# Performance work log

Measured on AMD Instinct MI355X. Metric: run time of the kernel, lower is better.

## Reference

```python
import jax, jax.numpy as jnp
import numpy as np

B, T, C = 4, 2048, 1024
H = 16
HD = C // H  # 64


def setup_inputs() -> dict:
    key = jax.random.key(0)
    k1, k2, k3 = jax.random.split(key, 3)
    x = jax.random.normal(k1, (B, T, C), dtype=jnp.float32)
    W_attn = jax.random.normal(k2, (C, 3 * C), dtype=jnp.float32) * (1.0 / np.sqrt(C))
    b_attn = jnp.zeros((3 * C,), dtype=jnp.float32)
    W_proj = jax.random.normal(k3, (C, C), dtype=jnp.float32) * (1.0 / np.sqrt(C))
    b_proj = jnp.zeros((C,), dtype=jnp.float32)
    return {"x": x, "W_attn": W_attn, "b_attn": b_attn, "W_proj": W_proj, "b_proj": b_proj}


def reference(x, W_attn, b_attn, W_proj, b_proj):
    Bx, Tx, Cx = x.shape
    qkv = x @ W_attn + b_attn                      # [B,T,3C]
    q, k, v = jnp.split(qkv, 3, axis=-1)
    # [B,T,C] -> [B,H,T,HD]
    q = q.reshape(Bx, Tx, H, HD).transpose(0, 2, 1, 3)
    k = k.reshape(Bx, Tx, H, HD).transpose(0, 2, 1, 3)
    v = v.reshape(Bx, Tx, H, HD).transpose(0, 2, 1, 3)
    att = jnp.einsum('bhqd,bhkd->bhqk', q, k) / jnp.sqrt(jnp.float32(HD))
    causal = jnp.tril(jnp.ones((Tx, Tx), dtype=bool))
    att = jnp.where(causal[None, None], att, -jnp.inf)
    att = jax.nn.softmax(att, axis=-1)
    y = jnp.einsum('bhqk,bhkd->bhqd', att, v)      # [B,H,T,HD]
    y = y.transpose(0, 2, 1, 3).reshape(Bx, Tx, Cx)
    return y @ W_proj + b_proj
```

## Files before the change

### kernel.cpp

```cpp
#include <hip/hip_runtime.h>
#include <hip/hip_bf16.h>

typedef unsigned short u16;
typedef __attribute__((ext_vector_type(8))) short bf16x8;
typedef __attribute__((ext_vector_type(4))) float f32x4;

#define MFMA16(a, b, c) __builtin_amdgcn_mfma_f32_16x16x32_bf16((a), (b), (c), 0, 0, 0)

__device__ __forceinline__ u16 f2bf(float f) {
  union { float f; unsigned u; } v; v.f = f;
  unsigned r = v.u + 0x7fffu + ((v.u >> 16) & 1u);
  return (u16)(r >> 16);
}

__device__ __forceinline__ unsigned pk_trunc(float hi, float lo) {
  union { float f; unsigned u; } a, b; a.f = hi; b.f = lo;
  return __builtin_amdgcn_perm(a.u, b.u, 0x07060302u);
}

__device__ __forceinline__ void gload_lds16(const u16* g, u16* l) {
  __builtin_amdgcn_global_load_lds((const __attribute__((address_space(1))) void*)g,
                                   (__attribute__((address_space(3))) void*)l, 16, 0, 0);
}

__global__ __launch_bounds__(256) void convert_bf16_k(const float* __restrict__ in,
                                                      u16* __restrict__ out, int n) {
  int i = (blockIdx.x * 256 + threadIdx.x) * 8;
  if (i >= n) return;
  float4 v0 = *(const float4*)(in + i);
  float4 v1 = *(const float4*)(in + i + 4);
  uint4 o;
  o.x = (unsigned)f2bf(v0.x) | ((unsigned)f2bf(v0.y) << 16);
  o.y = (unsigned)f2bf(v0.z) | ((unsigned)f2bf(v0.w) << 16);
  o.z = (unsigned)f2bf(v1.x) | ((unsigned)f2bf(v1.y) << 16);
  o.w = (unsigned)f2bf(v1.z) | ((unsigned)f2bf(v1.w) << 16);
  *(uint4*)(out + i) = o;
}

__global__ __launch_bounds__(256) void transpose2_k(const float* __restrict__ Wa, u16* __restrict__ WaT,
                                                    const float* __restrict__ Wp, u16* __restrict__ WpT) {
  __shared__ float tile[64][65];
  int b = blockIdx.x;
  const float* W; u16* Wt; int N, n0, k0;
  if (b < 768) { W = Wa; Wt = WaT; N = 3072; n0 = (b % 48) * 64; k0 = (b / 48) * 64; }
  else { int c = b - 768; W = Wp; Wt = WpT; N = 1024; n0 = (c & 15) * 64; k0 = (c >> 4) * 64; }
  const int tx = threadIdx.x & 63, ty = threadIdx.x >> 6;
#pragma unroll
  for (int i = 0; i < 16; ++i)
    tile[ty + 4 * i][tx] = W[(size_t)(k0 + ty + 4 * i) * N + n0 + tx];
  __syncthreads();
#pragma unroll
  for (int i = 0; i < 16; ++i)
    Wt[(size_t)(n0 + ty + 4 * i) * 1024 + k0 + tx] = f2bf(tile[tx][ty + 4 * i]);
}

#define BAR() asm volatile("s_barrier" ::: "memory")
#define WLG()                                                   \
  do {                                                          \
    asm volatile("s_waitcnt lgkmcnt(0)" ::: "memory");          \
    __builtin_amdgcn_sched_barrier(0);                          \
  } while (0)
#define VMW(N) asm volatile("s_waitcnt vmcnt(" #N ")" ::: "memory")

#define RING_LANE_CONSTS                                                    \
  const int tid = threadIdx.x, w = tid >> 6, lane = tid & 63;               \
  const int wm = w >> 2, wn = w & 3;                                        \
  const int fr = lane & 15, fg = lane >> 4;                                 \
  const int sr = lane >> 2;                                                 \
  const int sk = (lane & 1) * 8 + ((((lane >> 1) ^ (lane >> 5)) & 1) << 4); \
  const int lsw = fr * 32 + ((fg * 8) ^ ((fr & 8) ? 16 : 0));

__global__ __launch_bounds__(512, 2) void gemm_qkv_r4(const u16* __restrict__ A,
                                                      const u16* __restrict__ Bt,
                                                      const float* __restrict__ bias,
                                                      u16* __restrict__ Qo, u16* __restrict__ Ko,
                                                      u16* __restrict__ Vt) {
  __shared__ u16 sm[4][16384];
  const int bid = blockIdx.x;
  const int swz = (bid & 7) * 48 + (bid >> 3);
  const int m0 = (swz / 12) * 256, n0 = (swz % 12) * 256;
  RING_LANE_CONSTS
  const int aoff = wm * 4096 + lsw;
  const int boff = 8192 + wn * 2048 + lsw;

  const u16* gAw = A + (size_t)(m0 + sr) * 1024 + sk + (size_t)w * 16384;
  const u16* gBw = Bt + (size_t)(n0 + sr) * 1024 + sk + (size_t)w * 16384;

#define QSTG_A(SL, C, KO) \
  gload_lds16(gAw + (size_t)(C) * 131072 + (KO), &sm[SL][(C) * 4096 + w * 512 + lane * 8])
#define QSTG_B(SL, C, KO) \
  gload_lds16(gBw + (size_t)(C) * 131072 + (KO), &sm[SL][8192 + (C) * 4096 + w * 512 + lane * 8])

  f32x4 acc[8][4];
#pragma unroll
  for (int i = 0; i < 8; ++i)
#pragma unroll
    for (int j = 0; j < 4; ++j) acc[i][j] = (f32x4){0, 0, 0, 0};

  QSTG_A(0, 0, 0);  QSTG_B(0, 0, 0);  QSTG_A(0, 1, 0);  QSTG_B(0, 1, 0);
  QSTG_A(1, 0, 32); QSTG_B(1, 0, 32); QSTG_A(1, 1, 32); QSTG_B(1, 1, 32);
  QSTG_A(2, 0, 64); QSTG_B(2, 0, 64); QSTG_A(2, 1, 64); QSTG_B(2, 1, 64);
  int kofs = 96;
  VMW(8); BAR();

#define QLD_A(SL, M0_)                                                    \
  _Pragma("unroll") for (int i = 0; i < 4; ++i)                           \
      av[i] = *(const bf16x8*)&sm[SL][aoff + ((M0_) + i) * 512];
#define QLD_B(SL)                                                         \
  _Pragma("unroll") for (int i = 0; i < 4; ++i)                           \
      bv[i] = *(const bf16x8*)&sm[SL][boff + i * 512];
#define QMM(MB0)                                                          \
  __builtin_amdgcn_s_setprio(1);                                          \
  _Pragma("unroll") for (int i = 0; i < 4; ++i)                           \
      _Pragma("unroll") for (int j = 0; j < 4; ++j)                       \
          acc[(MB0) + i][j] = MFMA16(av[i], bv[j], acc[(MB0) + i][j]);    \
  __builtin_amdgcn_s_setprio(0);

#define QTILE(SL, SS, STG, CHK)                                                \
  {                                                                            \
    bf16x8 av[4], bv[4];                                                       \
    if (STG) { QSTG_A(SS, 0, kofs); QSTG_B(SS, 0, kofs);                       \
               QSTG_A(SS, 1, kofs); QSTG_B(SS, 1, kofs); }                     \
    QLD_A(SL, 0) QLD_B(SL)                                                     \
    WLG(); QMM(0)                                                              \
    QLD_A(SL, 4)                                                               \
    WLG(); QMM(4)                                                              \
    CHK;                                                                       \
    BAR();                                                                     \
    kofs += 32;                                                                \
  }

#pragma unroll 1
  for (int tp = 0; tp < 7; ++tp) {
    QTILE(0, 3, 1, VMW(8)) QTILE(1, 0, 1, VMW(8)) QTILE(2, 1, 1, VMW(8)) QTILE(3, 2, 1, VMW(8))
  }
  QTILE(0, 3, 1, VMW(8))
  QTILE(1, 0, 0, VMW(4))
  QTILE(2, 0, 0, VMW(0))
  QTILE(3, 0, 0, (void)0)

  const int which = n0 >> 10;
  if (which == 2) {
#pragma unroll
    for (int nb = 0; nb < 4; ++nb) {
      const int n = n0 + wn * 64 + nb * 16 + fr;
      const float bs = bias[n];
      const int c = n & 1023, h = c >> 6, hd = c & 63;
#pragma unroll
      for (int mb = 0; mb < 8; ++mb) {
        const int mbase = m0 + wm * 128 + mb * 16 + fg * 4;
        const int bb = mbase >> 11;
        const int tt = mbase & 2047;
        ushort4 pv;
        pv.x = f2bf(acc[mb][nb][0] + bs);
        pv.y = f2bf(acc[mb][nb][1] + bs);
        pv.z = f2bf(acc[mb][nb][2] + bs);
        pv.w = f2bf(acc[mb][nb][3] + bs);
        *(ushort4*)(Vt + ((size_t)(bb * 16 + h) * 64 + hd) * 2048 + tt) = pv;
      }
    }
  } else {
    u16* buf = &sm[0][0];
    const float sc = (which == 0) ? 0.125f : 1.0f;
    u16* outp = (which == 0) ? Qo : Ko;
    float bs4[4];
#pragma unroll
    for (int nb = 0; nb < 4; ++nb) bs4[nb] = bias[n0 + wn * 64 + nb * 16 + fr];
#pragma unroll
    for (int p = 0; p < 2; ++p) {
#pragma unroll
      for (int mb4 = 0; mb4 < 4; ++mb4) {
#pragma unroll
        for (int nb = 0; nb < 4; ++nb) {
#pragma unroll
          for (int r = 0; r < 4; ++r) {
            const int rl = wm * 64 + mb4 * 16 + fg * 4 + r;
            const int col = (wn * 64 + nb * 16 + fr) ^ ((rl & 7) << 3);
            buf[rl * 256 + col] = f2bf((acc[p * 4 + mb4][nb][r] + bs4[nb]) * sc);
          }
        }
      }
      BAR();
      {
        const int rl = tid >> 2, c4 = (tid & 3) * 64;
        const int m = m0 + (rl >> 6) * 128 + p * 64 + (rl & 63);
        const int bb = m >> 11, tt = m & 2047;
        const int n = n0 + c4;
        const int h = (n & 1023) >> 6;
        u16* dst = outp + ((size_t)(bb * 16 + h) * 2048 + tt) * 64;
#pragma unroll
        for (int i = 0; i < 8; ++i) {
          const int col = (c4 + i * 8) ^ ((rl & 7) << 3);
          *(uint4*)(dst + i * 8) = *(const uint4*)&buf[rl * 256 + col];
        }
      }
      BAR();
    }
  }
#undef QSTG_A
#undef QSTG_B
#undef QLD_A
#undef QLD_B
#undef QMM
#undef QTILE
}

__global__ __launch_bounds__(512, 2) void gemm_proj_r4(const u16* __restrict__ A,
                                                       const u16* __restrict__ Bt,
                                                       const float* __restrict__ bias,
                                                       float* __restrict__ O) {
  __shared__ u16 sm[4][12288];
  const int bid = blockIdx.x;
  const int swz = (bid & 7) * 32 + (bid >> 3);
  const int m0 = (swz >> 3) * 256, n0 = (swz & 7) * 128;
  RING_LANE_CONSTS
  const int aoff = wm * 4096 + lsw;
  const int boff = 8192 + wn * 1024 + lsw;

  const u16* gAw = A + (size_t)(m0 + sr) * 1024 + sk + (size_t)w * 16384;
  const u16* gBw = Bt + (size_t)(n0 + sr) * 1024 + sk + (size_t)w * 16384;

#define PSTG_A(SL, C, KO) \
  gload_lds16(gAw + (size_t)(C) * 131072 + (KO), &sm[SL][(C) * 4096 + w * 512 + lane * 8])
#define PSTG_B(SL, KO) \
  gload_lds16(gBw + (KO), &sm[SL][8192 + w * 512 + lane * 8])

  f32x4 acc[8][2];
#pragma unroll
  for (int i = 0; i < 8; ++i)
#pragma unroll
    for (int j = 0; j < 2; ++j) acc[i][j] = (f32x4){0, 0, 0, 0};

  PSTG_A(0, 0, 0);  PSTG_B(0, 0);  PSTG_A(0, 1, 0);
  PSTG_A(1, 0, 32); PSTG_B(1, 32); PSTG_A(1, 1, 32);
  PSTG_A(2, 0, 64); PSTG_B(2, 64); PSTG_A(2, 1, 64);
  int kofs = 96;
  VMW(6); BAR();

#define PLD_A(SL, M0_)                                                    \
  _Pragma("unroll") for (int i = 0; i < 4; ++i)                           \
      av[i] = *(const bf16x8*)&sm[SL][aoff + ((M0_) + i) * 512];
#define PLD_B(SL)                                                         \
  _Pragma("unroll") for (int i = 0; i < 2; ++i)                           \
      bv[i] = *(const bf16x8*)&sm[SL][boff + i * 512];
#define PMM(MB0)                                                          \
  __builtin_amdgcn_s_setprio(1);                                          \
  _Pragma("unroll") for (int i = 0; i < 4; ++i)                           \
      _Pragma("unroll") for (int j = 0; j < 2; ++j)                       \
          acc[(MB0) + i][j] = MFMA16(av[i], bv[j], acc[(MB0) + i][j]);    \
  __builtin_amdgcn_s_setprio(0);

#define PTILE(SL, SS, STG, CHK)                                                \
  {                                                                            \
    bf16x8 av[4], bv[2];                                                       \
    if (STG) { PSTG_A(SS, 0, kofs); PSTG_B(SS, kofs); PSTG_A(SS, 1, kofs); }   \
    PLD_A(SL, 0) PLD_B(SL)                                                     \
    WLG(); PMM(0)                                                              \
    PLD_A(SL, 4)                                                               \
    WLG(); PMM(4)                                                              \
    CHK;                                                                       \
    BAR();                                                                     \
    kofs += 32;                                                                \
  }

#pragma unroll 1
  for (int tp = 0; tp < 7; ++tp) {
    PTILE(0, 3, 1, VMW(6)) PTILE(1, 0, 1, VMW(6)) PTILE(2, 1, 1, VMW(6)) PTILE(3, 2, 1, VMW(6))
  }
  PTILE(0, 3, 1, VMW(6))
  PTILE(1, 0, 0, VMW(3))
  PTILE(2, 0, 0, VMW(0))
  PTILE(3, 0, 0, (void)0)

#pragma unroll
  for (int nb = 0; nb < 2; ++nb) {
    const int n = n0 + wn * 32 + nb * 16 + fr;
    const float bs = bias[n];
#pragma unroll
    for (int mb = 0; mb < 8; ++mb) {
      const int tg = m0 + wm * 128 + mb * 16 + fg * 4;
#pragma unroll
      for (int r = 0; r < 4; ++r) O[(size_t)(tg + r) * 1024 + n] = acc[mb][nb][r] + bs;
    }
  }
#undef PSTG_A
#undef PSTG_B
#undef PLD_A
#undef PLD_B
#undef PMM
#undef PTILE
}

#define PSTR 72
__global__ __launch_bounds__(256) void attn_k(const u16* __restrict__ Q,
                                              const u16* __restrict__ Kb,
                                              const u16* __restrict__ Vt,
                                              u16* __restrict__ Y) {
  __shared__ u16 Ks[64 * 72];
  __shared__ u16 Vs[64 * 72];
  __shared__ u16 Ps[4 * 32 * PSTR];
  const int L = blockIdx.x;
  const int xcd = L & 7, slot = L >> 3;
  const int bh = xcd * 8 + (slot & 7);
  const int i2 = slot >> 3;
  const int qt = (i2 & 4) ? ((i2 & 8) ? 4 + (i2 & 3) : (i2 & 3))
                          : ((i2 & 8) ? 11 - (i2 & 3) : 15 - (i2 & 3));
  const int tid = threadIdx.x, w = tid >> 6, lane = tid & 63;
  const int fr = lane & 15, fg = lane >> 4;
  const u16* Qp = Q + (size_t)bh * 2048 * 64;
  const u16* Kp = Kb + (size_t)bh * 2048 * 64;
  const u16* Vp = Vt + (size_t)bh * 64 * 2048;
  const int qw = qt * 128 + w * 32;

  bf16x8 qa[2][2];
#pragma unroll
  for (int g = 0; g < 2; ++g)
#pragma unroll
    for (int c = 0; c < 2; ++c)
      qa[g][c] = *(const bf16x8*)(Qp + (size_t)(qw + g * 16 + fr) * 64 + c * 32 + fg * 8);

  float li[2] = {0.f, 0.f};
  f32x4 ot[2][4];
#pragma unroll
  for (int g = 0; g < 2; ++g)
#pragma unroll
    for (int mb = 0; mb < 4; ++mb) ot[g][mb] = (f32x4){0, 0, 0, 0};

  const int srow = tid >> 2, scol = (tid & 3) * 16;
  u16* Pw = Ps + w * 32 * PSTR;
  const int nk = 2 * qt + 2;
  const u16* Kg = Kp + (size_t)srow * 64 + scol;
  const u16* Vg = Vp + (size_t)srow * 2048 + scol;

  uint4 kr0 = *(const uint4*)(Kg);
  uint4 kr1 = *(const uint4*)(Kg + 8);
  uint4 vr0 = *(const uint4*)(Vg);
  uint4 vr1 = *(const uint4*)(Vg + 8);

  for (int jt = 0; jt < nk; ++jt) {
    const int k0 = jt * 64;
    if (jt) __syncthreads();
    *(uint4*)&Ks[srow * 72 + scol] = kr0;
    *(uint4*)&Ks[srow * 72 + scol + 8] = kr1;
    *(uint4*)&Vs[srow * 72 + scol] = vr0;
    *(uint4*)&Vs[srow * 72 + scol + 8] = vr1;
    __syncthreads();
    if (jt + 1 < nk) {
      const int kn = (jt + 1) * 64;
      kr0 = *(const uint4*)(Kg + (size_t)kn * 64);
      kr1 = *(const uint4*)(Kg + (size_t)kn * 64 + 8);
      vr0 = *(const uint4*)(Vg + kn);
      vr1 = *(const uint4*)(Vg + kn + 8);
    }
    if (k0 > qw + 31) continue;

    bf16x8 kb[4][2];
#pragma unroll
    for (int nb = 0; nb < 4; ++nb) {
      kb[nb][0] = *(const bf16x8*)&Ks[(nb * 16 + fr) * 72 + fg * 8];
      kb[nb][1] = *(const bf16x8*)&Ks[(nb * 16 + fr) * 72 + 32 + fg * 8];
    }
    f32x4 st[2][4];
    __builtin_amdgcn_s_setprio(1);
#pragma unroll
    for (int g = 0; g < 2; ++g)
#pragma unroll
      for (int nb = 0; nb < 4; ++nb) {
        f32x4 z = (f32x4){0, 0, 0, 0};
        z = MFMA16(kb[nb][0], qa[g][0], z);
        z = MFMA16(kb[nb][1], qa[g][1], z);
        st[g][nb] = z;
      }
    __builtin_amdgcn_s_setprio(0);
    const bool needmask = (k0 + 63 > qw);
#pragma unroll
    for (int g = 0; g < 2; ++g) {
      const int q = qw + g * 16 + fr;
      float rs0 = 0.f, rs1 = 0.f;
#pragma unroll
      for (int nb = 0; nb < 4; ++nb) {
        const int kcb = k0 + nb * 16 + 4 * fg;
        float p0 = __expf(st[g][nb][0]);
        float p1 = __expf(st[g][nb][1]);
        float p2 = __expf(st[g][nb][2]);
        float p3 = __expf(st[g][nb][3]);
        if (needmask) {
          p0 = (kcb + 0 > q) ? 0.f : p0;
          p1 = (kcb + 1 > q) ? 0.f : p1;
          p2 = (kcb + 2 > q) ? 0.f : p2;
          p3 = (kcb + 3 > q) ? 0.f : p3;
        }
        rs0 += p0 + p1;
        rs1 += p2 + p3;
        *(uint2*)&Pw[(g * 16 + fr) * PSTR + nb * 16 + 4 * fg] =
            make_uint2(pk_trunc(p1, p0), pk_trunc(p3, p2));
      }
      li[g] += rs0 + rs1;
    }
    bf16x8 pa[2][2];
#pragma unroll
    for (int g = 0; g < 2; ++g)
#pragma unroll
      for (int H = 0; H < 2; ++H)
        pa[g][H] = *(const bf16x8*)&Pw[(g * 16 + fr) * PSTR + H * 32 + fg * 8];
    __builtin_amdgcn_s_setprio(1);
#pragma unroll
    for (int mb = 0; mb < 4; ++mb) {
      bf16x8 vb0 = *(const bf16x8*)&Vs[(mb * 16 + fr) * 72 + fg * 8];
      bf16x8 vb1 = *(const bf16x8*)&Vs[(mb * 16 + fr) * 72 + 32 + fg * 8];
#pragma unroll
      for (int g = 0; g < 2; ++g) {
        ot[g][mb] = MFMA16(vb0, pa[g][0], ot[g][mb]);
        ot[g][mb] = MFMA16(vb1, pa[g][1], ot[g][mb]);
      }
    }
    __builtin_amdgcn_s_setprio(0);
  }

  const int b = bh >> 4, h = bh & 15;
#pragma unroll
  for (int g = 0; g < 2; ++g) {
    float l = li[g];
    l += __shfl_xor(l, 16);
    l += __shfl_xor(l, 32);
    const float inv = 1.0f / l;
    const int t = qw + g * 16 + fr;
    u16* yrow = Y + ((size_t)b * 2048 + t) * 1024 + h * 64;
#pragma unroll
    for (int mb = 0; mb < 4; ++mb) {
      const unsigned d0 = (unsigned)f2bf(ot[g][mb][0] * inv) |
                          ((unsigned)f2bf(ot[g][mb][1] * inv) << 16);
      const unsigned d1 = (unsigned)f2bf(ot[g][mb][2] * inv) |
                          ((unsigned)f2bf(ot[g][mb][3] * inv) << 16);
      *(uint2*)&yrow[mb * 16 + fg * 4] = make_uint2(d0, d1);
    }
  }
}

extern "C" void kernel_launch(void* const* d_in, const int* in_sizes, int n_in,
                              void* d_out, int out_size, void* d_ws, size_t ws_size,
                              hipStream_t stream) {
  const float* x = (const float*)d_in[0];
  const float* Wa = (const float*)d_in[1];
  const float* ba = (const float*)d_in[2];
  const float* Wp = (const float*)d_in[3];
  const float* bp = (const float*)d_in[4];
  float* out = (float*)d_out;

  char* p = (char*)d_ws;
  u16* xb = (u16*)p;   p += (size_t)8192 * 1024 * 2;
  u16* WaT = (u16*)p;  p += (size_t)3072 * 1024 * 2;
  u16* WpT = (u16*)p;  p += (size_t)1024 * 1024 * 2;
  u16* Qb = (u16*)p;   p += (size_t)64 * 2048 * 64 * 2;
  u16* Kbuf = (u16*)p; p += (size_t)64 * 2048 * 64 * 2;
  u16* Vtb = (u16*)p;  p += (size_t)64 * 64 * 2048 * 2;
  u16* Yb = (u16*)p;   p += (size_t)8192 * 1024 * 2;

  convert_bf16_k<<<4096, 256, 0, stream>>>(x, xb, 8192 * 1024);
  transpose2_k<<<1024, 256, 0, stream>>>(Wa, WaT, Wp, WpT);
  gemm_qkv_r4<<<384, 512, 0, stream>>>(xb, WaT, ba, Qb, Kbuf, Vtb);
  attn_k<<<1024, 256, 0, stream>>>(Qb, Kbuf, Vtb, Yb);
  gemm_proj_r4<<<256, 512, 0, stream>>>(Yb, WpT, bp, out);
}
```

Measured before the change: 240.6 us.

## Retile QKV GEMM to 128x256 blocks with 4 waves and 3-stage ring

The QKV projection GEMM moves from 256x256 tiles with 8 waves and a 4-slot LDS ring to 128x256 tiles with 4 waves, each wave covering a 128x64 strip, and a 3-slot ring. The grid grows from 384 to 768 blocks to improve load balance across CUs, and LDS per block shrinks so more blocks can be resident. The epilogue is simplified to a single LDS staging pass. The cost is lower data reuse per block, since each block now loads more bytes per FLOP, plus a shallower prefetch ring.

```diff
diff --git a/kernel.cpp b/kernel.cpp
--- a/kernel.cpp
+++ b/kernel.cpp
@@ -62,34 +62,29 @@
   } while (0)
 #define VMW(N) asm volatile("s_waitcnt vmcnt(" #N ")" ::: "memory")
 
-#define RING_LANE_CONSTS                                                    \
-  const int tid = threadIdx.x, w = tid >> 6, lane = tid & 63;               \
-  const int wm = w >> 2, wn = w & 3;                                        \
-  const int fr = lane & 15, fg = lane >> 4;                                 \
-  const int sr = lane >> 2;                                                 \
-  const int sk = (lane & 1) * 8 + ((((lane >> 1) ^ (lane >> 5)) & 1) << 4); \
-  const int lsw = fr * 32 + ((fg * 8) ^ ((fr & 8) ? 16 : 0));
-
-__global__ __launch_bounds__(512, 2) void gemm_qkv_r4(const u16* __restrict__ A,
+__global__ __launch_bounds__(256, 2) void gemm_qkv_cr(const u16* __restrict__ A,
                                                       const u16* __restrict__ Bt,
                                                       const float* __restrict__ bias,
                                                       u16* __restrict__ Qo, u16* __restrict__ Ko,
                                                       u16* __restrict__ Vt) {
-  __shared__ u16 sm[4][16384];
+  __shared__ u16 sm[3][12288];
   const int bid = blockIdx.x;
-  const int swz = (bid & 7) * 48 + (bid >> 3);
-  const int m0 = (swz / 12) * 256, n0 = (swz % 12) * 256;
-  RING_LANE_CONSTS
-  const int aoff = wm * 4096 + lsw;
-  const int boff = 8192 + wn * 2048 + lsw;
-
-  const u16* gAw = A + (size_t)(m0 + sr) * 1024 + sk + (size_t)w * 16384;
-  const u16* gBw = Bt + (size_t)(n0 + sr) * 1024 + sk + (size_t)w * 16384;
-
-#define QSTG_A(SL, C, KO) \
-  gload_lds16(gAw + (size_t)(C) * 131072 + (KO), &sm[SL][(C) * 4096 + w * 512 + lane * 8])
-#define QSTG_B(SL, C, KO) \
-  gload_lds16(gBw + (size_t)(C) * 131072 + (KO), &sm[SL][8192 + (C) * 4096 + w * 512 + lane * 8])
+  const int swz = (bid & 7) * 96 + (bid >> 3);
+  const int m0 = (swz / 12) * 128, n0 = (swz % 12) * 256;
+  const int tid = threadIdx.x, w = tid >> 6, lane = tid & 63;
+  const int fr = lane & 15, fg = lane >> 4;
+  const int sk = (tid & 1) * 8 + ((((tid >> 1) ^ (tid >> 5)) & 1) << 4);
+  const int lsw = fr * 32 + ((fg * 8) ^ ((fr & 8) ? 16 : 0));
+  const int aoff = lsw;
+  const int boff = 4096 + w * 2048 + lsw;
+
+  const u16* gA = A + (size_t)(m0 + (tid >> 2)) * 1024 + sk;
+  const u16* gB = Bt + (size_t)(n0 + (tid >> 2)) * 1024 + sk;
+
+#define QSTG_A(SL, C) \
+  gload_lds16(gA + (size_t)(C) * 65536 + kofs, &sm[SL][(C) * 2048 + tid * 8])
+#define QSTG_B(SL, C) \
+  gload_lds16(gB + (size_t)(C) * 65536 + kofs, &sm[SL][4096 + (C) * 2048 + tid * 8])
 
   f32x4 acc[8][4];
 #pragma unroll
@@ -97,11 +92,14 @@
 #pragma unroll
     for (int j = 0; j < 4; ++j) acc[i][j] = (f32x4){0, 0, 0, 0};
 
-  QSTG_A(0, 0, 0);  QSTG_B(0, 0, 0);  QSTG_A(0, 1, 0);  QSTG_B(0, 1, 0);
-  QSTG_A(1, 0, 32); QSTG_B(1, 0, 32); QSTG_A(1, 1, 32); QSTG_B(1, 1, 32);
-  QSTG_A(2, 0, 64); QSTG_B(2, 0, 64); QSTG_A(2, 1, 64); QSTG_B(2, 1, 64);
-  int kofs = 96;
-  VMW(8); BAR();
+  int kofs = 0;
+  QSTG_A(0, 0); QSTG_A(0, 1);
+  QSTG_B(0, 0); QSTG_B(0, 1); QSTG_B(0, 2); QSTG_B(0, 3);
+  kofs = 32;
+  QSTG_A(1, 0); QSTG_A(1, 1);
+  QSTG_B(1, 0); QSTG_B(1, 1); QSTG_B(1, 2); QSTG_B(1, 3);
+  kofs = 64;
+  VMW(6); BAR();
 
 #define QLD_A(SL, M0_)                                                    \
   _Pragma("unroll") for (int i = 0; i < 4; ++i)                           \
@@ -119,8 +117,8 @@
 #define QTILE(SL, SS, STG, CHK)                                                \
   {                                                                            \
     bf16x8 av[4], bv[4];                                                       \
-    if (STG) { QSTG_A(SS, 0, kofs); QSTG_B(SS, 0, kofs);                       \
-               QSTG_A(SS, 1, kofs); QSTG_B(SS, 1, kofs); }                     \
+    if (STG) { QSTG_A(SS, 0); QSTG_A(SS, 1);                                   \
+               QSTG_B(SS, 0); QSTG_B(SS, 1); QSTG_B(SS, 2); QSTG_B(SS, 3); }   \
     QLD_A(SL, 0) QLD_B(SL)                                                     \
     WLG(); QMM(0)                                                              \
     QLD_A(SL, 4)                                                               \
@@ -131,24 +129,22 @@
   }
 
 #pragma unroll 1
-  for (int tp = 0; tp < 7; ++tp) {
-    QTILE(0, 3, 1, VMW(8)) QTILE(1, 0, 1, VMW(8)) QTILE(2, 1, 1, VMW(8)) QTILE(3, 2, 1, VMW(8))
-  }
-  QTILE(0, 3, 1, VMW(8))
-  QTILE(1, 0, 0, VMW(4))
-  QTILE(2, 0, 0, VMW(0))
-  QTILE(3, 0, 0, (void)0)
+  for (int tp = 0; tp < 10; ++tp) {
+    QTILE(0, 2, 1, VMW(6)) QTILE(1, 0, 1, VMW(6)) QTILE(2, 1, 1, VMW(6))
+  }
+  QTILE(0, 0, 0, VMW(0))
+  QTILE(1, 0, 0, (void)0)
 
   const int which = n0 >> 10;
   if (which == 2) {
 #pragma unroll
     for (int nb = 0; nb < 4; ++nb) {
-      const int n = n0 + wn * 64 + nb * 16 + fr;
+      const int n = n0 + w * 64 + nb * 16 + fr;
       const float bs = bias[n];
       const int c = n & 1023, h = c >> 6, hd = c & 63;
 #pragma unroll
       for (int mb = 0; mb < 8; ++mb) {
-        const int mbase = m0 + wm * 128 + mb * 16 + fg * 4;
+        const int mbase = m0 + mb * 16 + fg * 4;
         const int bb = mbase >> 11;
         const int tt = mbase & 2047;
         ushort4 pv;
@@ -165,36 +161,33 @@
     u16* outp = (which == 0) ? Qo : Ko;
     float bs4[4];
 #pragma unroll
-    for (int nb = 0; nb < 4; ++nb) bs4[nb] = bias[n0 + wn * 64 + nb * 16 + fr];
-#pragma unroll
-    for (int p = 0; p < 2; ++p) {
-#pragma unroll
-      for (int mb4 = 0; mb4 < 4; ++mb4) {
-#pragma unroll
-        for (int nb = 0; nb < 4; ++nb) {
-#pragma unroll
-          for (int r = 0; r < 4; ++r) {
-            const int rl = wm * 64 + mb4 * 16 + fg * 4 + r;
-            const int col = (wn * 64 + nb * 16 + fr) ^ ((rl & 7) << 3);
-            buf[rl * 256 + col] = f2bf((acc[p * 4 + mb4][nb][r] + bs4[nb]) * sc);
-          }
+    for (int nb = 0; nb < 4; ++nb) bs4[nb] = bias[n0 + w * 64 + nb * 16 + fr];
+#pragma unroll
+    for (int mb = 0; mb < 8; ++mb) {
+#pragma unroll
+      for (int nb = 0; nb < 4; ++nb) {
+#pragma unroll
+        for (int r = 0; r < 4; ++r) {
+          const int rl = mb * 16 + fg * 4 + r;
+          const int col = (w * 64 + nb * 16 + fr) ^ ((rl & 7) << 3);
+          buf[rl * 256 + col] = f2bf((acc[mb][nb][r] + bs4[nb]) * sc);
         }
       }
-      BAR();
-      {
-        const int rl = tid >> 2, c4 = (tid & 3) * 64;
-        const int m = m0 + (rl >> 6) * 128 + p * 64 + (rl & 63);
-        const int bb = m >> 11, tt = m & 2047;
-        const int n = n0 + c4;
-        const int h = (n & 1023) >> 6;
-        u16* dst = outp + ((size_t)(bb * 16 + h) * 2048 + tt) * 64;
-#pragma unroll
-        for (int i = 0; i < 8; ++i) {
-          const int col = (c4 + i * 8) ^ ((rl & 7) << 3);
-          *(uint4*)(dst + i * 8) = *(const uint4*)&buf[rl * 256 + col];
-        }
-      }
-      BAR();
+    }
+    BAR();
+#pragma unroll
+    for (int p2 = 0; p2 < 2; ++p2) {
+      const int rl = p2 * 64 + (tid >> 2), c4 = (tid & 3) * 64;
+      const int m = m0 + rl;
+      const int bb = m >> 11, tt = m & 2047;
+      const int n = n0 + c4;
+      const int h = (n & 1023) >> 6;
+      u16* dst = outp + ((size_t)(bb * 16 + h) * 2048 + tt) * 64;
+#pragma unroll
+      for (int i = 0; i < 8; ++i) {
+        const int col = (c4 + i * 8) ^ ((rl & 7) << 3);
+        *(uint4*)(dst + i * 8) = *(const uint4*)&buf[rl * 256 + col];
+      }
     }
   }
 #undef QSTG_A
@@ -204,6 +197,14 @@
 #undef QMM
 #undef QTILE
 }
+
+#define RING_LANE_CONSTS                                                    \
+  const int tid = threadIdx.x, w = tid >> 6, lane = tid & 63;               \
+  const int wm = w >> 2, wn = w & 3;                                        \
+  const int fr = lane & 15, fg = lane >> 4;                                 \
+  const int sr = lane >> 2;                                                 \
+  const int sk = (lane & 1) * 8 + ((((lane >> 1) ^ (lane >> 5)) & 1) << 4); \
+  const int lsw = fr * 32 + ((fg * 8) ^ ((fr & 8) ? 16 : 0));
 
 __global__ __launch_bounds__(512, 2) void gemm_proj_r4(const u16* __restrict__ A,
                                                        const u16* __restrict__ Bt,
@@ -458,7 +459,7 @@
 
   convert_bf16_k<<<4096, 256, 0, stream>>>(x, xb, 8192 * 1024);
   transpose2_k<<<1024, 256, 0, stream>>>(Wa, WaT, Wp, WpT);
-  gemm_qkv_r4<<<384, 512, 0, stream>>>(xb, WaT, ba, Qb, Kbuf, Vtb);
+  gemm_qkv_cr<<<768, 256, 0, stream>>>(xb, WaT, ba, Qb, Kbuf, Vtb);
   attn_k<<<1024, 256, 0, stream>>>(Qb, Kbuf, Vtb, Yb);
   gemm_proj_r4<<<256, 512, 0, stream>>>(Yb, WpT, bp, out);
 }
```

Measured after the change: 242.9 us. No clear change (+1.0%).
